# Kernel optimization log

Hardware: AMD Instinct MI355X
Metric: run time of the kernel (lower is better)

Reference implementation:

```python
import jax, jax.numpy as jnp
import numpy as np

B, D, NH, HD = 32, 384, 8, 48
HP = WP = 14
N = HP * WP
L = 24
EPS_LN = 1e-5


def _ln(x, w, b):
    m = jnp.mean(x, -1, keepdims=True)
    v = jnp.mean((x - m) ** 2, -1, keepdims=True)
    return (x - m) * jax.lax.rsqrt(v + EPS_LN) * w + b


def _gelu(x):
    return jax.nn.gelu(x, approximate=False)


def _conv(x, w, s, p, groups=1):
    return jax.lax.conv_general_dilated(x, w, (s, s), [(p, p), (p, p)],
        dimension_numbers=('NCHW', 'OIHW', 'NCHW'), feature_group_count=groups)


def _bn(x, g, b):
    # eval-mode BatchNorm2d with running_mean=0, running_var=1
    scale = g * jax.lax.rsqrt(jnp.asarray(1.0 + 1e-5, x.dtype))
    return x * scale[None, :, None, None] + b[None, :, None, None]


def _pos_embed(pos_w, pos_b):
    two_pi = 2.0 * np.pi
    y = (jnp.arange(HP, dtype=jnp.float32) + 1.0) / ((HP + 1e-6) * two_pi)
    xg = (jnp.arange(WP, dtype=jnp.float32) + 1.0) / ((WP + 1e-6) * two_pi)
    y_embed = jnp.broadcast_to(y[:, None], (HP, WP))
    x_embed = jnp.broadcast_to(xg[None, :], (HP, WP))
    dim_t = 10000.0 ** (2.0 * (jnp.arange(32) // 2).astype(jnp.float32) / 32.0)
    px = x_embed[..., None] / dim_t  # [H,W,32]
    py = y_embed[..., None] / dim_t
    px = jnp.stack([jnp.sin(px[..., 0::2]), jnp.cos(px[..., 1::2])], -1).reshape(HP, WP, 32)
    py = jnp.stack([jnp.sin(py[..., 0::2]), jnp.cos(py[..., 1::2])], -1).reshape(HP, WP, 32)
    pos = jnp.concatenate([py, px], -1)  # [H,W,64]
    pos = jnp.einsum('hwc,dc->hwd', pos, pos_w[:, :, 0, 0]) + pos_b
    return pos.reshape(1, N, D)


def _xca_block(t, p):
    Bc = t.shape[0]
    h = _ln(t, p['n1_w'], p['n1_b'])
    qkv = (h @ p['qkv_w'].T + p['qkv_b']).reshape(Bc, N, 3, NH, HD)
    q = qkv[:, :, 0].transpose(0, 2, 3, 1)  # [B,H,d,N]
    k = qkv[:, :, 1].transpose(0, 2, 3, 1)
    v = qkv[:, :, 2].transpose(0, 2, 3, 1)
    q = q / jnp.maximum(jnp.linalg.norm(q, axis=-1, keepdims=True), 1e-12)
    k = k / jnp.maximum(jnp.linalg.norm(k, axis=-1, keepdims=True), 1e-12)
    attn = jnp.einsum('bhdn,bhen->bhde', q, k) * p['temp'][None, :, None, None]
    a = jax.nn.softmax(attn, -1)  # channel-wise softmax over d_h
    o = jnp.einsum('bhde,bhen->bnhd', a, v).reshape(Bc, N, D)
    o = o @ p['proj_w'].T + p['proj_b']
    t = t + p['g1'] * o
    h = _ln(t, p['n3_w'], p['n3_b']).transpose(0, 2, 1).reshape(Bc, D, HP, WP)
    h = _conv(h, p['lpi1_w'], 1, 1, groups=D) + p['lpi1_b'][None, :, None, None]
    h = _bn(_gelu(h), p['lpi_bn_g'], p['lpi_bn_b'])
    h = _conv(h, p['lpi2_w'], 1, 1, groups=D) + p['lpi2_b'][None, :, None, None]
    t = t + p['g3'] * h.reshape(Bc, D, N).transpose(0, 2, 1)
    h = _ln(t, p['n2_w'], p['n2_b'])
    h = _gelu(h @ p['fc1_w'].T + p['fc1_b']) @ p['fc2_w'].T + p['fc2_b']
    return t + p['g2'] * h


def _ca_block(t, p):
    Bc, Nc, _ = t.shape
    h = _ln(t, p['n1_w'], p['n1_b'])
    qkv = (h @ p['qkv_w'].T + p['qkv_b']).reshape(Bc, Nc, 3, NH, HD)
    q = qkv[:, :, 0].transpose(0, 2, 1, 3)  # [B,H,N,d]
    k = qkv[:, :, 1].transpose(0, 2, 1, 3)
    v = qkv[:, :, 2].transpose(0, 2, 1, 3)
    attn = jnp.sum(q[:, :, :1] * k, -1) * (HD ** -0.5)  # [B,H,N]
    a = jax.nn.softmax(attn, -1)
    cls = jnp.einsum('bhn,bhnd->bhd', a, v).reshape(Bc, 1, D)
    cls = cls @ p['proj_w'].T + p['proj_b']
    attn_out = jnp.concatenate([cls, h[:, 1:]], 1)
    t = t + p['g1'] * attn_out
    t = _ln(t, p['n2_w'], p['n2_b'])
    res = t
    cls2 = _gelu(t[:, :1] @ p['fc1_w'].T + p['fc1_b']) @ p['fc2_w'].T + p['fc2_b']
    return jnp.concatenate([p['g2'] * cls2, t[:, 1:]], 1) + res


def setup_inputs() -> dict:
    key = jax.random.key(0)
    k = iter(jax.random.split(key, 64))
    def rn(shape, std=0.02):
        return jax.random.normal(next(k), shape, jnp.float32) * std
    inp = {}
    inp['x'] = jax.random.normal(next(k), (B, 3, 224, 224), jnp.float32)
    inp['cls_token'] = rn((1, 1, D))
    inp['pos_w'] = rn((D, 64, 1, 1))
    inp['pos_b'] = jnp.zeros((D,))
    for i, (co, ci) in enumerate([(48, 3), (96, 48), (192, 96), (384, 192)], 1):
        inp['pe_w%d' % i] = rn((co, ci, 3, 3))
        inp['pe_g%d' % i] = jnp.ones((co,))
        inp['pe_b%d' % i] = jnp.zeros((co,))
    inp['xqkv_w'] = rn((L, 3 * D, D)); inp['xqkv_b'] = jnp.zeros((L, 3 * D))
    inp['xproj_w'] = rn((L, D, D)); inp['xproj_b'] = jnp.zeros((L, D))
    inp['xtemp'] = jnp.ones((L, NH))
    for n in ('n1', 'n2', 'n3'):
        inp['x%s_w' % n] = jnp.ones((L, D)); inp['x%s_b' % n] = jnp.zeros((L, D))
    inp['xfc1_w'] = rn((L, 4 * D, D)); inp['xfc1_b'] = jnp.zeros((L, 4 * D))
    inp['xfc2_w'] = rn((L, D, 4 * D)); inp['xfc2_b'] = jnp.zeros((L, D))
    inp['xlpi1_w'] = rn((L, D, 1, 3, 3), 0.1); inp['xlpi1_b'] = jnp.zeros((L, D))
    inp['xlpi2_w'] = rn((L, D, 1, 3, 3), 0.1); inp['xlpi2_b'] = jnp.zeros((L, D))
    inp['xbn_g'] = jnp.ones((L, D)); inp['xbn_b'] = jnp.zeros((L, D))
    for g in ('g1', 'g2', 'g3'):
        inp['x%s' % g] = jnp.full((L, D), 1e-5)
    L2 = 2
    inp['cqkv_w'] = rn((L2, 3 * D, D)); inp['cqkv_b'] = jnp.zeros((L2, 3 * D))
    inp['cproj_w'] = rn((L2, D, D)); inp['cproj_b'] = jnp.zeros((L2, D))
    for n in ('n1', 'n2'):
        inp['c%s_w' % n] = jnp.ones((L2, D)); inp['c%s_b' % n] = jnp.zeros((L2, D))
    inp['cfc1_w'] = rn((L2, 4 * D, D)); inp['cfc1_b'] = jnp.zeros((L2, 4 * D))
    inp['cfc2_w'] = rn((L2, D, 4 * D)); inp['cfc2_b'] = jnp.zeros((L2, D))
    inp['cg1'] = jnp.full((L2, D), 1e-5); inp['cg2'] = jnp.full((L2, D), 1e-5)
    inp['norm_w'] = jnp.ones((D,)); inp['norm_b'] = jnp.zeros((D,))
    inp['head_w'] = rn((1000, D)); inp['head_b'] = jnp.zeros((1000,))
    return inp


def reference(x, cls_token, pos_w, pos_b, pe_w1, pe_g1, pe_b1, pe_w2, pe_g2, pe_b2, pe_w3, pe_g3, pe_b3, pe_w4, pe_g4, pe_b4, xqkv_w, xqkv_b, xproj_w, xproj_b, xtemp, xn1_w, xn1_b, xn2_w, xn2_b, xn3_w, xn3_b, xfc1_w, xfc1_b, xfc2_w, xfc2_b, xlpi1_w, xlpi1_b, xlpi2_w, xlpi2_b, xbn_g, xbn_b, xg1, xg2, xg3, cqkv_w, cqkv_b, cproj_w, cproj_b, cn1_w, cn1_b, cn2_w, cn2_b, cfc1_w, cfc1_b, cfc2_w, cfc2_b, cg1, cg2, norm_w, norm_b, head_w, head_b):
    h = _gelu(_bn(_conv(x, pe_w1, 2, 1), pe_g1, pe_b1))
    h = _gelu(_bn(_conv(h, pe_w2, 2, 1), pe_g2, pe_b2))
    h = _gelu(_bn(_conv(h, pe_w3, 2, 1), pe_g3, pe_b3))
    h = _bn(_conv(h, pe_w4, 2, 1), pe_g4, pe_b4)  # [B,D,14,14]
    t = h.reshape(h.shape[0], D, N).transpose(0, 2, 1)  # [B,N,D]
    t = t + _pos_embed(pos_w, pos_b)
    xca = {'qkv_w': xqkv_w, 'qkv_b': xqkv_b, 'proj_w': xproj_w, 'proj_b': xproj_b,
           'temp': xtemp, 'n1_w': xn1_w, 'n1_b': xn1_b, 'n2_w': xn2_w, 'n2_b': xn2_b,
           'n3_w': xn3_w, 'n3_b': xn3_b, 'fc1_w': xfc1_w, 'fc1_b': xfc1_b,
           'fc2_w': xfc2_w, 'fc2_b': xfc2_b, 'lpi1_w': xlpi1_w, 'lpi1_b': xlpi1_b,
           'lpi2_w': xlpi2_w, 'lpi2_b': xlpi2_b, 'lpi_bn_g': xbn_g, 'lpi_bn_b': xbn_b,
           'g1': xg1, 'g2': xg2, 'g3': xg3}
    t, _ = jax.lax.scan(lambda c, p: (_xca_block(c, p), None), t, xca)
    t = jnp.concatenate([jnp.broadcast_to(cls_token, (t.shape[0], 1, D)), t], 1)
    for i in range(2):
        p = {'qkv_w': cqkv_w[i], 'qkv_b': cqkv_b[i], 'proj_w': cproj_w[i],
             'proj_b': cproj_b[i], 'n1_w': cn1_w[i], 'n1_b': cn1_b[i],
             'n2_w': cn2_w[i], 'n2_b': cn2_b[i], 'fc1_w': cfc1_w[i],
             'fc1_b': cfc1_b[i], 'fc2_w': cfc2_w[i], 'fc2_b': cfc2_b[i],
             'g1': cg1[i], 'g2': cg2[i]}
        t = _ca_block(t, p)
    t = _ln(t, norm_w, norm_b)[:, 0]
    return t @ head_w.T + head_b
```

## Files before the change

kernel.cpp:

```cpp
#include <hip/hip_runtime.h>
#include <hip/hip_bf16.h>

#define B_ 32
#define D_ 384
#define N_ 196
#define NH_ 8
#define HD_ 48
#define L_ 24

typedef __bf16 bf16x8 __attribute__((ext_vector_type(8)));
typedef float f32x4 __attribute__((ext_vector_type(4)));

__device__ __forceinline__ float gelu_f(float v){
    return 0.5f * v * (1.0f + erff(v * 0.70710678118654752f));
}

__global__ __launch_bounds__(256) void cvt_bf(const float* __restrict__ s, __bf16* __restrict__ d, long n){
    long i = ((long)blockIdx.x * 256 + threadIdx.x) * 8;
    if (i >= n) return;
    float4 a = *reinterpret_cast<const float4*>(s + i);
    float4 b = *reinterpret_cast<const float4*>(s + i + 4);
    bf16x8 r;
    r[0] = (__bf16)a.x; r[1] = (__bf16)a.y; r[2] = (__bf16)a.z; r[3] = (__bf16)a.w;
    r[4] = (__bf16)b.x; r[5] = (__bf16)b.y; r[6] = (__bf16)b.z; r[7] = (__bf16)b.w;
    *reinterpret_cast<bf16x8*>(d + i) = r;
}

__global__ __launch_bounds__(256) void cvt_pad(const float* __restrict__ s, __bf16* __restrict__ d,
                                               int rows, int K, int rows_pad){
    int id = blockIdx.x * 256 + threadIdx.x;
    if (id >= rows_pad * K) return;
    int r = id / K;
    d[id] = (r < rows) ? (__bf16)s[id] : (__bf16)0.f;
}

__global__ __launch_bounds__(256) void wprep(const float* __restrict__ w, __bf16* __restrict__ W2,
                                             int Co, int Ci, int Kpad){
    int id = blockIdx.x * 256 + threadIdx.x;
    if (id >= Co * Kpad) return;
    int co = id / Kpad, k = id - co * Kpad;
    float v = 0.f;
    if (k < 9 * Ci){
        int tap = k / Ci, ci = k - tap * Ci;
// ... 153 lines not shown
    float* yr = y + row * ystride;
    yr[tid]       = (v0 - m) * r * w[tid]       + b[tid];
    yr[tid + 128] = (v1 - m) * r * w[tid + 128] + b[tid + 128];
    yr[tid + 256] = (v2 - m) * r * w[tid + 256] + b[tid + 256];
}

__global__ __launch_bounds__(128) void ln384_bf(const float* __restrict__ x,
                                                const float* __restrict__ w, const float* __restrict__ b,
                                                __bf16* __restrict__ y){
    long row = blockIdx.x;
    int tid = threadIdx.x;
    const float* xr = x + row * 384;
    float v0 = xr[tid], v1 = xr[tid + 128], v2 = xr[tid + 256];
    float s = v0 + v1 + v2;
    float ss = v0 * v0 + v1 * v1 + v2 * v2;
    for (int off = 32; off; off >>= 1){ s += __shfl_down(s, off); ss += __shfl_down(ss, off); }
    __shared__ float rs[2], rss[2];
    if ((tid & 63) == 0){ rs[tid >> 6] = s; rss[tid >> 6] = ss; }
    __syncthreads();
    float S = rs[0] + rs[1], SS = rss[0] + rss[1];
    float m = S * (1.0f / 384.0f);
    float var = SS * (1.0f / 384.0f) - m * m;
    float r = rsqrtf(var + 1e-5f);
    __bf16* yr = y + row * 384;
    yr[tid]       = (__bf16)((v0 - m) * r * w[tid]       + b[tid]);
    yr[tid + 128] = (__bf16)((v1 - m) * r * w[tid + 128] + b[tid + 128]);
    yr[tid + 256] = (__bf16)((v2 - m) * r * w[tid + 256] + b[tid + 256]);
}

__global__ __launch_bounds__(128) void proj_res_lnt(const __bf16* __restrict__ o2,
                                                    const float* __restrict__ g1,
                                                    float* __restrict__ t,
                                                    const float* __restrict__ n3w, const float* __restrict__ n3b,
                                                    float* __restrict__ ht){
    long row = blockIdx.x;
    int tid = threadIdx.x;
    float v[3];
    #pragma unroll
    for (int i = 0; i < 3; i++){
        int c = tid + i * 128;
        long idx = row * 384 + c;
        v[i] = t[idx] + g1[c] * (float)o2[idx];
        t[idx] = v[i];
    }
    float s = v[0] + v[1] + v[2];
    float ss = v[0] * v[0] + v[1] * v[1] + v[2] * v[2];
    for (int off = 32; off; off >>= 1){ s += __shfl_down(s, off); ss += __shfl_down(ss, off); }
    __shared__ float rs[2], rss[2];
    if ((tid & 63) == 0){ rs[tid >> 6] = s; rss[tid >> 6] = ss; }
    __syncthreads();
    float S = rs[0] + rs[1], SS = rss[0] + rss[1];
    float m = S * (1.0f / 384.0f);
    float var = SS * (1.0f / 384.0f) - m * m;
    float r = rsqrtf(var + 1e-5f);
    int b = (int)(row / 196), n = (int)(row % 196);
    float* yb = ht + ((long)b * 384) * 196 + n;
    #pragma unroll
    for (int i = 0; i < 3; i++){
        int c = tid + i * 128;
        yb[(long)c * 196] = (v[i] - m) * r * n3w[c] + n3b[c];
    }
}

__global__ __launch_bounds__(128) void ln2res(float* __restrict__ t,
                                              const __bf16* __restrict__ hadd,
                                              const float* __restrict__ n2w, const float* __restrict__ n2b,
                                              __bf16* __restrict__ h){
    long row = blockIdx.x;
    int tid = threadIdx.x;
    float v[3];
    #pragma unroll
    for (int i = 0; i < 3; i++){
        int c = tid + i * 128;
        long idx = row * 384 + c;
        v[i] = t[idx] + (float)hadd[idx];
        t[idx] = v[i];
    }
    float s = v[0] + v[1] + v[2];
    float ss = v[0] * v[0] + v[1] * v[1] + v[2] * v[2];
    for (int off = 32; off; off >>= 1){ s += __shfl_down(s, off); ss += __shfl_down(ss, off); }
    __shared__ float rs[2], rss[2];
    if ((tid & 63) == 0){ rs[tid >> 6] = s; rss[tid >> 6] = ss; }
    __syncthreads();
    float S = rs[0] + rs[1], SS = rss[0] + rss[1];
    float m = S * (1.0f / 384.0f);
    float var = SS * (1.0f / 384.0f) - m * m;
    float r = rsqrtf(var + 1e-5f);
    __bf16* yr = h + row * 384;
    #pragma unroll
    for (int i = 0; i < 3; i++){
        int c = tid + i * 128;
        yr[c] = (__bf16)((v[i] - m) * r * n2w[c] + n2b[c]);
    }
}

__global__ __launch_bounds__(128) void fc2_res_ln(const __bf16* __restrict__ f2,
                                                  const float* __restrict__ g2,
                                                  float* __restrict__ t,
                                                  const float* __restrict__ n1w, const float* __restrict__ n1b,
                                                  __bf16* __restrict__ h){
    long row = blockIdx.x;
    int tid = threadIdx.x;
    float v[3];
    #pragma unroll
    for (int i = 0; i < 3; i++){
        int c = tid + i * 128;
        long idx = row * 384 + c;
        v[i] = t[idx] + g2[c] * (float)f2[idx];
        t[idx] = v[i];
    }
    float s = v[0] + v[1] + v[2];
    float ss = v[0] * v[0] + v[1] * v[1] + v[2] * v[2];
    for (int off = 32; off; off >>= 1){ s += __shfl_down(s, off); ss += __shfl_down(ss, off); }
    __shared__ float rs[2], rss[2];
    if ((tid & 63) == 0){ rs[tid >> 6] = s; rss[tid >> 6] = ss; }
    __syncthreads();
    float S = rs[0] + rs[1], SS = rss[0] + rss[1];
    float m = S * (1.0f / 384.0f);
    float var = SS * (1.0f / 384.0f) - m * m;
    float r = rsqrtf(var + 1e-5f);
    __bf16* yr = h + row * 384;
    #pragma unroll
    for (int i = 0; i < 3; i++){
        int c = tid + i * 128;
        yr[c] = (__bf16)((v[i] - m) * r * n1w[c] + n1b[c]);
    }
}

template<int MODE, int OUTBF, int ACVT, int GUARD, int SPLITK, int NGUARD>
__global__ __launch_bounds__(256) void gemm_bb2(const void* __restrict__ Av, long lda,
                                                const __bf16* __restrict__ W, int Kw,
                                                const float* __restrict__ bias,
                                                void* __restrict__ Cv, long ldc,
                                                int K, int M, int Ncols){
    __shared__ __align__(16) char smem[15360];
    char* Ab = smem;
    char* Bb = smem + 5120;
    const int tid = threadIdx.x;
    const int lane = tid & 63;
    const int wn = tid >> 6;
    const int row0 = blockIdx.x * 64;
    const int col0 = blockIdx.y * 128;
    const int hi = lane >> 4, lo = lane & 15;
    const int kbase = SPLITK ? blockIdx.z * K : 0;
    const __bf16* Abf = (const __bf16*)Av;
    const float* Af = (const float*)Av;
    const int r_a = tid >> 2, cq_a = tid & 3;
    f32x4 acc[4][2] = {};
    auto loadA = [&](int kk)->bf16x8 {
        bf16x8 va{};
        int grow = row0 + r_a;
        if (!GUARD || grow < M){
            long ai = (long)grow * lda + kk + cq_a * 8;
            if (ACVT){
                float4 a0 = *reinterpret_cast<const float4*>(Af + ai);
                float4 a1 = *reinterpret_cast<const float4*>(Af + ai + 4);
                va[0] = (__bf16)a0.x; va[1] = (__bf16)a0.y; va[2] = (__bf16)a0.z; va[3] = (__bf16)a0.w;
                va[4] = (__bf16)a1.x; va[5] = (__bf16)a1.y; va[6] = (__bf16)a1.z; va[7] = (__bf16)a1.w;
            } else {
                va = *reinterpret_cast<const bf16x8*>(Abf + ai);
            }
        }
        return va;
    };
    auto loadB = [&](int kk, int i)->bf16x8 {
        int p = i * 256 + tid;
        int r = p >> 2, cq = p & 3;
        return *reinterpret_cast<const bf16x8*>(W + (long)(col0 + r) * Kw + kk + cq * 8);
    };
    bf16x8 vaC = loadA(kbase);
    bf16x8 vwC0 = loadB(kbase, 0), vwC1 = loadB(kbase, 1);
    for (int k0 = 0; k0 < K; k0 += 32){
        *reinterpret_cast<bf16x8*>(Ab + r_a * 80 + cq_a * 16) = vaC;
        #pragma unroll
        for (int i = 0; i < 2; i++){
            int p = i * 256 + tid;
            int r = p >> 2, cq = p & 3;
            *reinterpret_cast<bf16x8*>(Bb + r * 80 + cq * 16) = i ? vwC1 : vwC0;
        }
        __syncthreads();
        int kn = kbase + ((k0 + 32 < K) ? k0 + 32 : k0);
        bf16x8 vaN = loadA(kn);
        bf16x8 vwN0 = loadB(kn, 0), vwN1 = loadB(kn, 1);
        bf16x8 af[4], bfr[2];
        #pragma unroll
        for (int m = 0; m < 4; m++)
            af[m] = *reinterpret_cast<const bf16x8*>(Ab + (m * 16 + lo) * 80 + hi * 16);
        #pragma unroll
        for (int n = 0; n < 2; n++)
            bfr[n] = *reinterpret_cast<const bf16x8*>(Bb + (wn * 32 + n * 16 + lo) * 80 + hi * 16);
        #pragma unroll
        for (int m = 0; m < 4; m++)
            #pragma unroll
            for (int n = 0; n < 2; n++)
                acc[m][n] = __builtin_amdgcn_mfma_f32_16x16x32_bf16(af[m], bfr[n], acc[m][n], 0, 0, 0);
        __syncthreads();
        vaC = vaN; vwC0 = vwN0; vwC1 = vwN1;
    }
    float* Cf = (float*)Cv;
    __bf16* Cb = (__bf16*)Cv;
    if (SPLITK) Cf += (long)blockIdx.z * M * ldc;
    #pragma unroll
    for (int m = 0; m < 4; m++){
        #pragma unroll
        for (int n = 0; n < 2; n++){
            int row = row0 + m * 16 + hi * 4;
            int col = col0 + wn * 32 + n * 16 + lo;
            if (NGUARD && col >= Ncols) continue;
            float bv = (MODE == 3) ? 0.f : bias[col];
            #pragma unroll
            for (int j = 0; j < 4; j++){
                if (GUARD && (row + j) >= M) continue;
                float v = acc[m][n][j] + bv;
                if (MODE == 1) v = gelu_f(v);
                long ci = (long)(row + j) * ldc + col;
                if (OUTBF) Cb[ci] = (__bf16)v;
                else Cf[ci] = v;
            }
        }
    }
}

__global__ __launch_bounds__(256) void gemm_bb3(const __bf16* __restrict__ A, long lda,
                                                const __bf16* __restrict__ W, int Kw,
                                                const float* __restrict__ bias,
                                                __bf16* __restrict__ C, long ldc,
                                                int K){
    __shared__ __align__(16) char smem[10240];
    char* Ab = smem;
    char* Bb = smem + 5120;
    const int tid = threadIdx.x;
    const int lane = tid & 63;
    const int wn = tid >> 6;
    const int row0 = blockIdx.x * 64;
    const int col0 = blockIdx.y * 64;
    const int hi = lane >> 4, lo = lane & 15;
    const int r_s = tid >> 2, cq_s = tid & 3;
    f32x4 acc[4] = {};
    auto loadA = [&](int kk)->bf16x8 {
        return *reinterpret_cast<const bf16x8*>(A + (long)(row0 + r_s) * lda + kk + cq_s * 8);
    };
    auto loadB = [&](int kk)->bf16x8 {
        return *reinterpret_cast<const bf16x8*>(W + (long)(col0 + r_s) * Kw + kk + cq_s * 8);
    };
    bf16x8 vaC = loadA(0);
    bf16x8 vwC = loadB(0);
    for (int k0 = 0; k0 < K; k0 += 32){
        *reinterpret_cast<bf16x8*>(Ab + r_s * 80 + cq_s * 16) = vaC;
        *reinterpret_cast<bf16x8*>(Bb + r_s * 80 + cq_s * 16) = vwC;
        __syncthreads();
        int kn = (k0 + 32 < K) ? k0 + 32 : k0;
        bf16x8 vaN = loadA(kn);
        bf16x8 vwN = loadB(kn);
        bf16x8 af[4], bfr;
        #pragma unroll
        for (int m = 0; m < 4; m++)
            af[m] = *reinterpret_cast<const bf16x8*>(Ab + (m * 16 + lo) * 80 + hi * 16);
        bfr = *reinterpret_cast<const bf16x8*>(Bb + (wn * 16 + lo) * 80 + hi * 16);
        #pragma unroll
        for (int m = 0; m < 4; m++)
            acc[m] = __builtin_amdgcn_mfma_f32_16x16x32_bf16(af[m], bfr, acc[m], 0, 0, 0);
        __syncthreads();
        vaC = vaN; vwC = vwN;
    }
    #pragma unroll
    for (int m = 0; m < 4; m++){
        int row = row0 + m * 16 + hi * 4;
        int col = col0 + wn * 16 + lo;
        float bv = bias[col];
        #pragma unroll
        for (int j = 0; j < 4; j++)
            C[(long)(row + j) * ldc + col] = (__bf16)(acc[m][j] + bv);
    }
}

__global__ __launch_bounds__(384) void pos_embed(const float* __restrict__ pw, const float* __restrict__ pb,
                                                 float* __restrict__ pos){
    __shared__ float p64[64];
    int n = blockIdx.x;
    int iy = n / 14, ix = n % 14;
    int t = threadIdx.x;
    if (t < 64){
        int axis = t >> 5;
        int c = t & 31;
        int u = c >> 1;
        float coord = (axis == 0) ? (float)(iy + 1) : (float)(ix + 1);
        float val = coord / ((14.0f + 1e-6f) * 6.283185307179586f);
        float T = powf(10000.0f, (float)u / 16.0f);
        float a = val / T;
        p64[t] = (c & 1) ? cosf(a) : sinf(a);
    }
    __syncthreads();
    float acc = 0.f;
    const float* wr = pw + (long)t * 64;
    #pragma unroll 8
    for (int c = 0; c < 64; c++) acc += p64[c] * wr[c];
// ... 131 lines not shown
        sm += __shfl_xor(sm, 2);
        float inv = 1.0f / sm;
        #pragma unroll
        for (int i = 0; i < 12; i++) abf[r * 72 + q4 * 12 + i] = (__bf16)(pv[i] * inv);
    }
    for (int idx = tid; idx < 48 * 3; idx += 256){
        int r = idx / 3, c = 48 + (idx % 3) * 8;
        *reinterpret_cast<bf16x8*>(abf + r * 72 + c) = z8;
    }
    __syncthreads();
    __bf16* ob = o + ((long)b * 196) * 384 + h * 48;
    __builtin_amdgcn_s_setprio(1);
    for (int tt = wid; tt < 39; tt += 4){
        int mi = tt / 13, ni = tt % 13;
        f32x4 acc = {};
        #pragma unroll
        for (int e0 = 0; e0 < 64; e0 += 32){
            bf16x8 af = *reinterpret_cast<const bf16x8*>(abf + (mi * 16 + lo) * 72 + e0 + hi * 8);
            bf16x8 bf = *reinterpret_cast<const bf16x8*>(vt + (ni * 16 + lo) * 72 + e0 + hi * 8);
            acc = __builtin_amdgcn_mfma_f32_16x16x32_bf16(af, bf, acc, 0, 0, 0);
        }
        int n = ni * 16 + lo;
        if (n < 196){
            #pragma unroll
            for (int j = 0; j < 4; j++){
                int d = mi * 16 + hi * 4 + j;
                ob[(long)n * 384 + d] = (__bf16)acc[j];
            }
        }
    }
    __builtin_amdgcn_s_setprio(0);
}

__global__ __launch_bounds__(256) void lpi_g(const float* __restrict__ ht,
                                             const float* __restrict__ w1, const float* __restrict__ b1,
                                             const float* __restrict__ bng, const float* __restrict__ bnb,
                                             const float* __restrict__ w2, const float* __restrict__ b2,
                                             const float* __restrict__ g3, __bf16* __restrict__ hadd){
    int bd = blockIdx.x;
    int d = bd % 384, b = bd / 384;
    __shared__ float p[16][16];
    __shared__ float p2[16][16];
    __shared__ float wA[9], wB[9];
    int tt = threadIdx.x;
    int yy = tt / 16, xx = tt % 16;
    p[yy][xx] = 0.f; p2[yy][xx] = 0.f;
    if (tt < 9){ wA[tt] = w1[d * 9 + tt]; wB[tt] = w2[d * 9 + tt]; }
    __syncthreads();
    if (tt < 196){
        int y = tt / 14, x = tt % 14;
        p[y + 1][x + 1] = ht[((long)b * 384 + d) * 196 + tt];
    }
    __syncthreads();
    if (tt < 196){
        int y = tt / 14, x = tt % 14;
        float a = 0.f;
        #pragma unroll
        for (int ky = 0; ky < 3; ky++)
            #pragma unroll
            for (int kx = 0; kx < 3; kx++)
                a += wA[ky * 3 + kx] * p[y + ky][x + kx];
        a += b1[d];
        a = gelu_f(a);
        a = a * (bng[d] * rsqrtf(1.0f + 1e-5f)) + bnb[d];
        p2[y + 1][x + 1] = a;
    }
    __syncthreads();
    if (tt < 196){
        int y = tt / 14, x = tt % 14;
        float a = 0.f;
        #pragma unroll
        for (int ky = 0; ky < 3; ky++)
            #pragma unroll
            for (int kx = 0; kx < 3; kx++)
                a += wB[ky * 3 + kx] * p2[y + ky][x + kx];
        a += b2[d];
        hadd[((long)b * 196 + tt) * 384 + d] = (__bf16)(g3[d] * a);
    }
}

__global__ __launch_bounds__(256) void concat_cls(const float* __restrict__ t, const float* __restrict__ clstok,
                                                  float* __restrict__ tc){
    long i = (long)blockIdx.x * 256 + threadIdx.x;
    if (i >= (long)B_ * 197 * 384) return;
// ... 114 lines not shown
    const float* cfc1_b = (const float*)d_in[49];
    const float* cfc2_w = (const float*)d_in[50];
    const float* cfc2_b = (const float*)d_in[51];
    const float* cg1 = (const float*)d_in[52];
    const float* cg2 = (const float*)d_in[53];
    const float* norm_w = (const float*)d_in[54];
    const float* norm_b = (const float*)d_in[55];
    const float* head_w = (const float*)d_in[56];
    const float* head_b = (const float*)d_in[57];
    float* outp = (float*)d_out;

    float* ws = (float*)d_ws;
    __bf16* A1   = (__bf16*)(ws);
    __bf16* A2   = (__bf16*)(ws);
    __bf16* A3   = (__bf16*)(ws);
    __bf16* A4   = (__bf16*)(ws);
    __bf16* out1 = (__bf16*)(ws + 22500000L);
    __bf16* out2 = (__bf16*)(ws + 22500000L);
    __bf16* out3 = (__bf16*)(ws + 27400000L);
    __bf16* wcv  = (__bf16*)(ws + 36000000L);
    __bf16* W1c = wcv;
    __bf16* W2c = wcv + 1536;
    __bf16* W3c = wcv + 44544;
    __bf16* W4c = wcv + 216576;
    __bf16* wqkv_bf = (__bf16*)(ws);
    __bf16* wproj_bf = (__bf16*)(ws + 5308416L);
    __bf16* wfc1_bf = (__bf16*)(ws + 7077888L);
    __bf16* wfc2_bf = (__bf16*)(ws + 14155776L);
    float*  t       = ws + 21233664L;
    float*  pos     = ws + 23642112L;
    __bf16* h_bf    = (__bf16*)(ws + 23717376L);
    __bf16* qkv_bf  = (__bf16*)(ws + 24921600L);
    __bf16* o_bf    = (__bf16*)(ws + 28534272L);
    float*  ht      = ws + 29738496L;
    __bf16* f1_bf   = (__bf16*)(ws + 32146944L);
    __bf16* o2_bf   = (__bf16*)(ws + 34555392L);
    __bf16* f2_bf   = (__bf16*)(ws + 24921600L);
    __bf16* hadd_bf = (__bf16*)(ws + 28534272L);
    float* tc   = ws;
    float* hc   = ws + 2420736L;
    __bf16* qkvc_bf = (__bf16*)(ws + 4841472L);
    float* clsp = ws + 8472576L;
    float* clso = clsp + 12288;
    float* f1c  = clso + 12288;
    float* cls2 = f1c + 49152;
    float* clsf = cls2 + 12288;
    __bf16* cqkv_bf  = (__bf16*)(ws + 9000000L);
    __bf16* cproj_bf = (__bf16*)(ws + 9500000L);
    __bf16* cfc1_bf  = (__bf16*)(ws + 9800000L);
    __bf16* cfc2_bf  = (__bf16*)(ws + 10400000L);
    __bf16* headw_bf = (__bf16*)(ws + 11000000L);

    wprep<<<(48 * 32 + 255) / 256, 256, 0, stream>>>(pe_w[0], W1c, 48, 3, 32);
    wprep<<<(96 * 448 + 255) / 256, 256, 0, stream>>>(pe_w[1], W2c, 96, 48, 448);
    wprep<<<(192 * 896 + 255) / 256, 256, 0, stream>>>(pe_w[2], W3c, 192, 96, 896);
    wprep<<<(384 * 1728 + 255) / 256, 256, 0, stream>>>(pe_w[3], W4c, 384, 192, 1728);

    im2col_x<<<1568, 256, 0, stream>>>(x, A1);
    { dim3 g(3136, 1); gemm_conv<1, 0><<<g, 256, 0, stream>>>(A1, 32, W1c, pe_g[0], pe_b[0], out1, 48, nullptr); }
    im2col_bf<<<(100352 * 9 + 255) / 256, 256, 0, stream>>>(out1, A2, 48, 112, 112, 56, 56, 448, 100352 * 9);
    { dim3 g(784, 1); gemm_conv<1, 0><<<g, 256, 0, stream>>>(A2, 448, W2c, pe_g[1], pe_b[1], out2, 96, nullptr); }
    im2col_bf<<<(25088 * 9 + 255) / 256, 256, 0, stream>>>(out2, A3, 96, 56, 56, 28, 28, 896, 25088 * 9);
    pos_embed<<<196, 384, 0, stream>>>(pos_w, pos_b, pos);
    { dim3 g(196, 2); gemm_conv<1, 0><<<g, 256, 0, stream>>>(A3, 896, W3c, pe_g[2], pe_b[2], out3, 192, nullptr); }
    im2col_bf<<<(6272 * 9 + 255) / 256, 256, 0, stream>>>(out3, A4, 192, 28, 28, 14, 14, 1728, 6272 * 9);
    { dim3 g(49, 3); gemm_conv<0, 1><<<g, 256, 0, stream>>>(A4, 1728, W4c, pe_g[3], pe_b[3], t, 384, pos); }

    {
        long n1 = (long)L_ * 1152 * 384;
        long n2 = (long)L_ * 384 * 384;
        long n3 = (long)L_ * 1536 * 384;
        cvt_bf<<<(int)((n1 + 2047) / 2048), 256, 0, stream>>>(xqkv_w, wqkv_bf, n1);
        cvt_bf<<<(int)((n2 + 2047) / 2048), 256, 0, stream>>>(xproj_w, wproj_bf, n2);
        cvt_bf<<<(int)((n3 + 2047) / 2048), 256, 0, stream>>>(xfc1_w, wfc1_bf, n3);
        cvt_bf<<<(int)((n3 + 2047) / 2048), 256, 0, stream>>>(xfc2_w, wfc2_bf, n3);
    }

    const int M = B_ * N_;
    ln384_bf<<<M, 128, 0, stream>>>(t, xn1_w, xn1_b, h_bf);
    for (int l = 0; l < L_; l++){
        {
            dim3 g(98, 9);
            gemm_bb2<0, 1, 0, 0, 0, 0><<<g, 256, 0, stream>>>(h_bf, 384, wqkv_bf + (long)l * 1152 * 384, 384,
                                                              xqkv_b + l * 1152, qkv_bf, 1152, 384, M, 0);
        }
        xca2<<<B_ * NH_, 256, 0, stream>>>(qkv_bf, xtemp + l * 8, o_bf);
        {
            dim3 g(98, 6);
            gemm_bb3<<<g, 256, 0, stream>>>(o_bf, 384, wproj_bf + (long)l * 384 * 384, 384,
                                            xproj_b + l * 384, o2_bf, 384, 384);
        }
        proj_res_lnt<<<M, 128, 0, stream>>>(o2_bf, xg1 + l * 384, t,
                                            xn3_w + l * 384, xn3_b + l * 384, ht);
        lpi_g<<<B_ * D_, 256, 0, stream>>>(ht, xlpi1_w + (long)l * 384 * 9, xlpi1_b + l * 384,
                                           xbn_g + l * 384, xbn_b + l * 384,
                                           xlpi2_w + (long)l * 384 * 9, xlpi2_b + l * 384,
                                           xg3 + l * 384, hadd_bf);
        ln2res<<<M, 128, 0, stream>>>(t, hadd_bf, xn2_w + l * 384, xn2_b + l * 384, h_bf);
        {
            dim3 g(98, 12);
            gemm_bb2<1, 1, 0, 0, 0, 0><<<g, 256, 0, stream>>>(h_bf, 384, wfc1_bf + (long)l * 1536 * 384, 384,
                                                              xfc1_b + l * 1536, f1_bf, 1536, 384, M, 0);
        }
        {
            dim3 g(98, 6);
            gemm_bb3<<<g, 256, 0, stream>>>(f1_bf, 1536, wfc2_bf + (long)l * 1536 * 384, 1536,
                                            xfc2_b + l * 384, f2_bf, 384, 1536);
        }
        int ln = (l + 1) % L_;
        fc2_res_ln<<<M, 128, 0, stream>>>(f2_bf, xg2 + l * 384, t,
                                          xn1_w + ln * 384, xn1_b + ln * 384, h_bf);
    }

    const long NC = (long)B_ * 197 * 384;
    concat_cls<<<(int)(NC / 256), 256, 0, stream>>>(t, clstok, tc);
    {
        long nc = (long)2 * 1152 * 384;
        cvt_bf<<<(int)((nc + 2047) / 2048), 256, 0, stream>>>(cqkv_w, cqkv_bf, nc);
        long np = (long)2 * 384 * 384;
        cvt_bf<<<(int)((np + 2047) / 2048), 256, 0, stream>>>(cproj_w, cproj_bf, np);
        long nf = (long)2 * 1536 * 384;
        cvt_bf<<<(int)((nf + 2047) / 2048), 256, 0, stream>>>(cfc1_w, cfc1_bf, nf);
        cvt_bf<<<(int)((nf + 2047) / 2048), 256, 0, stream>>>(cfc2_w, cfc2_bf, nf);
        cvt_pad<<<(1024 * 384 + 255) / 256, 256, 0, stream>>>(head_w, headw_bf, 1000, 384, 1024);
    }
    const int MC = B_ * 197;
    for (int i = 0; i < 2; i++){
        ln384<<<MC, 128, 0, stream>>>(tc, 384, cn1_w + i * 384, cn1_b + i * 384, hc, 384);
        {
            dim3 g(99, 9);
            gemm_bb2<0, 1, 1, 1, 0, 0><<<g, 256, 0, stream>>>(hc, 384, cqkv_bf + (long)i * 1152 * 384, 384,
                                                              cqkv_b + i * 1152, qkvc_bf, 1152, 384, MC, 0);
        }
        ca_attn<<<B_ * NH_, 256, 0, stream>>>(qkvc_bf, clsp);
        {
            dim3 g(1, 3);
            gemm_bb2<0, 0, 1, 1, 0, 0><<<g, 256, 0, stream>>>(clsp, 384, cproj_bf + (long)i * 384 * 384, 384,
                                                              cproj_b + i * 384, clso, 384, 384, 32, 0);
        }
        ca_update1<<<(int)(NC / 256), 256, 0, stream>>>(clso, hc, cg1 + i * 384, tc);
        ln384<<<MC, 128, 0, stream>>>(tc, 384, cn2_w + i * 384, cn2_b + i * 384, hc, 384);
        {
            dim3 g(1, 12);
            gemm_bb2<1, 0, 1, 1, 0, 0><<<g, 256, 0, stream>>>(hc, (long)197 * 384, cfc1_bf + (long)i * 1536 * 384, 384,
                                                              cfc1_b + i * 1536, f1c, 1536, 384, 32, 0);
        }
        {
            dim3 g(1, 3);
            gemm_bb2<0, 0, 1, 1, 0, 0><<<g, 256, 0, stream>>>(f1c, 1536, cfc2_bf + (long)i * 1536 * 384, 1536,
                                                              cfc2_b + i * 384, cls2, 384, 1536, 32, 0);
        }
        ca_update2<<<(int)(NC / 256), 256, 0, stream>>>(cls2, hc, cg2 + i * 384, tc);
    }

    ln384<<<32, 128, 0, stream>>>(tc, (long)197 * 384, norm_w, norm_b, clsf, 384);
    {
        dim3 g(1, 8);
        gemm_bb2<0, 0, 1, 1, 0, 1><<<g, 256, 0, stream>>>(clsf, 384, headw_bf, 384,
                                                          head_b, outp, 1000, 384, 32, 1000);
    }
}
```

Measured before the change: 4.188 ms.

## Double GEMM K-tile to 64, vectorize LN kernels, store LPI input as bf16

```diff
diff --git a/kernel.cpp b/kernel.cpp
--- a/kernel.cpp
+++ b/kernel.cpp
@@ -9,6 +9,7 @@
 #define L_ 24
 
 typedef __bf16 bf16x8 __attribute__((ext_vector_type(8)));
+typedef __bf16 bf16x4 __attribute__((ext_vector_type(4)));
 typedef float f32x4 __attribute__((ext_vector_type(4)));
 
 __device__ __forceinline__ float gelu_f(float v){
@@ -228,19 +229,22 @@
                                                     const float* __restrict__ g1,
                                                     float* __restrict__ t,
                                                     const float* __restrict__ n3w, const float* __restrict__ n3b,
-                                                    float* __restrict__ ht){
+                                                    __bf16* __restrict__ ht){
     long row = blockIdx.x;
     int tid = threadIdx.x;
-    float v[3];
-    #pragma unroll
-    for (int i = 0; i < 3; i++){
-        int c = tid + i * 128;
-        long idx = row * 384 + c;
-        v[i] = t[idx] + g1[c] * (float)o2[idx];
-        t[idx] = v[i];
-    }
-    float s = v[0] + v[1] + v[2];
-    float ss = v[0] * v[0] + v[1] * v[1] + v[2] * v[2];
+    int c0 = tid * 4;
+    float v[4] = {0.f, 0.f, 0.f, 0.f};
+    if (tid < 96){
+        float4 tv = *reinterpret_cast<const float4*>(t + row * 384 + c0);
+        bf16x4 ov = *reinterpret_cast<const bf16x4*>(o2 + row * 384 + c0);
+        v[0] = tv.x + g1[c0 + 0] * (float)ov[0];
+        v[1] = tv.y + g1[c0 + 1] * (float)ov[1];
+        v[2] = tv.z + g1[c0 + 2] * (float)ov[2];
+        v[3] = tv.w + g1[c0 + 3] * (float)ov[3];
+        *reinterpret_cast<float4*>(t + row * 384 + c0) = make_float4(v[0], v[1], v[2], v[3]);
+    }
+    float s = v[0] + v[1] + v[2] + v[3];
+    float ss = v[0] * v[0] + v[1] * v[1] + v[2] * v[2] + v[3] * v[3];
     for (int off = 32; off; off >>= 1){ s += __shfl_down(s, off); ss += __shfl_down(ss, off); }
     __shared__ float rs[2], rss[2];
     if ((tid & 63) == 0){ rs[tid >> 6] = s; rss[tid >> 6] = ss; }
@@ -249,12 +253,14 @@
     float m = S * (1.0f / 384.0f);
     float var = SS * (1.0f / 384.0f) - m * m;
     float r = rsqrtf(var + 1e-5f);
-    int b = (int)(row / 196), n = (int)(row % 196);
-    float* yb = ht + ((long)b * 384) * 196 + n;
-    #pragma unroll
-    for (int i = 0; i < 3; i++){
-        int c = tid + i * 128;
-        yb[(long)c * 196] = (v[i] - m) * r * n3w[c] + n3b[c];
+    if (tid < 96){
+        int b = (int)(row / 196), n = (int)(row % 196);
+        __bf16* yb = ht + ((long)b * 384) * 196 + n;
+        #pragma unroll
+        for (int j = 0; j < 4; j++){
+            int c = c0 + j;
+            yb[(long)c * 196] = (__bf16)((v[j] - m) * r * n3w[c] + n3b[c]);
+        }
     }
 }
 
@@ -264,16 +270,19 @@
                                               __bf16* __restrict__ h){
     long row = blockIdx.x;
     int tid = threadIdx.x;
-    float v[3];
-    #pragma unroll
-    for (int i = 0; i < 3; i++){
-        int c = tid + i * 128;
-        long idx = row * 384 + c;
-        v[i] = t[idx] + (float)hadd[idx];
-        t[idx] = v[i];
-    }
-    float s = v[0] + v[1] + v[2];
-    float ss = v[0] * v[0] + v[1] * v[1] + v[2] * v[2];
+    int c0 = tid * 4;
+    float v[4] = {0.f, 0.f, 0.f, 0.f};
+    if (tid < 96){
+        float4 tv = *reinterpret_cast<const float4*>(t + row * 384 + c0);
+        bf16x4 hv = *reinterpret_cast<const bf16x4*>(hadd + row * 384 + c0);
+        v[0] = tv.x + (float)hv[0];
+        v[1] = tv.y + (float)hv[1];
+        v[2] = tv.z + (float)hv[2];
+        v[3] = tv.w + (float)hv[3];
+        *reinterpret_cast<float4*>(t + row * 384 + c0) = make_float4(v[0], v[1], v[2], v[3]);
+    }
+    float s = v[0] + v[1] + v[2] + v[3];
+    float ss = v[0] * v[0] + v[1] * v[1] + v[2] * v[2] + v[3] * v[3];
     for (int off = 32; off; off >>= 1){ s += __shfl_down(s, off); ss += __shfl_down(ss, off); }
     __shared__ float rs[2], rss[2];
     if ((tid & 63) == 0){ rs[tid >> 6] = s; rss[tid >> 6] = ss; }
@@ -282,11 +291,14 @@
     float m = S * (1.0f / 384.0f);
     float var = SS * (1.0f / 384.0f) - m * m;
     float r = rsqrtf(var + 1e-5f);
-    __bf16* yr = h + row * 384;
-    #pragma unroll
-    for (int i = 0; i < 3; i++){
-        int c = tid + i * 128;
-        yr[c] = (__bf16)((v[i] - m) * r * n2w[c] + n2b[c]);
+    if (tid < 96){
+        bf16x4 o;
+        #pragma unroll
+        for (int j = 0; j < 4; j++){
+            int c = c0 + j;
+            o[j] = (__bf16)((v[j] - m) * r * n2w[c] + n2b[c]);
+        }
+        *reinterpret_cast<bf16x4*>(h + row * 384 + c0) = o;
     }
 }
 
@@ -297,16 +309,19 @@
                                                   __bf16* __restrict__ h){
     long row = blockIdx.x;
     int tid = threadIdx.x;
-    float v[3];
-    #pragma unroll
-    for (int i = 0; i < 3; i++){
-        int c = tid + i * 128;
-        long idx = row * 384 + c;
-        v[i] = t[idx] + g2[c] * (float)f2[idx];
-        t[idx] = v[i];
-    }
-    float s = v[0] + v[1] + v[2];
-    float ss = v[0] * v[0] + v[1] * v[1] + v[2] * v[2];
+    int c0 = tid * 4;
+    float v[4] = {0.f, 0.f, 0.f, 0.f};
+    if (tid < 96){
+        float4 tv = *reinterpret_cast<const float4*>(t + row * 384 + c0);
+        bf16x4 fv = *reinterpret_cast<const bf16x4*>(f2 + row * 384 + c0);
+        v[0] = tv.x + g2[c0 + 0] * (float)fv[0];
+        v[1] = tv.y + g2[c0 + 1] * (float)fv[1];
+        v[2] = tv.z + g2[c0 + 2] * (float)fv[2];
+        v[3] = tv.w + g2[c0 + 3] * (float)fv[3];
+        *reinterpret_cast<float4*>(t + row * 384 + c0) = make_float4(v[0], v[1], v[2], v[3]);
+    }
+    float s = v[0] + v[1] + v[2] + v[3];
+    float ss = v[0] * v[0] + v[1] * v[1] + v[2] * v[2] + v[3] * v[3];
     for (int off = 32; off; off >>= 1){ s += __shfl_down(s, off); ss += __shfl_down(ss, off); }
     __shared__ float rs[2], rss[2];
     if ((tid & 63) == 0){ rs[tid >> 6] = s; rss[tid >> 6] = ss; }
@@ -315,39 +330,42 @@
     float m = S * (1.0f / 384.0f);
     float var = SS * (1.0f / 384.0f) - m * m;
     float r = rsqrtf(var + 1e-5f);
-    __bf16* yr = h + row * 384;
-    #pragma unroll
-    for (int i = 0; i < 3; i++){
-        int c = tid + i * 128;
-        yr[c] = (__bf16)((v[i] - m) * r * n1w[c] + n1b[c]);
-    }
-}
-
-template<int MODE, int OUTBF, int ACVT, int GUARD, int SPLITK, int NGUARD>
+    if (tid < 96){
+        bf16x4 o;
+        #pragma unroll
+        for (int j = 0; j < 4; j++){
+            int c = c0 + j;
+            o[j] = (__bf16)((v[j] - m) * r * n1w[c] + n1b[c]);
+        }
+        *reinterpret_cast<bf16x4*>(h + row * 384 + c0) = o;
+    }
+}
+
+template<int MODE, int OUTBF, int ACVT, int GUARD, int NGUARD>
 __global__ __launch_bounds__(256) void gemm_bb2(const void* __restrict__ Av, long lda,
                                                 const __bf16* __restrict__ W, int Kw,
                                                 const float* __restrict__ bias,
                                                 void* __restrict__ Cv, long ldc,
                                                 int K, int M, int Ncols){
-    __shared__ __align__(16) char smem[15360];
+    __shared__ __align__(16) char smem[27648];
     char* Ab = smem;
-    char* Bb = smem + 5120;
+    char* Bb = smem + 9216;
     const int tid = threadIdx.x;
     const int lane = tid & 63;
     const int wn = tid >> 6;
     const int row0 = blockIdx.x * 64;
     const int col0 = blockIdx.y * 128;
     const int hi = lane >> 4, lo = lane & 15;
-    const int kbase = SPLITK ? blockIdx.z * K : 0;
     const __bf16* Abf = (const __bf16*)Av;
     const float* Af = (const float*)Av;
-    const int r_a = tid >> 2, cq_a = tid & 3;
     f32x4 acc[4][2] = {};
-    auto loadA = [&](int kk)->bf16x8 {
+    auto loadA = [&](int kk, int i)->bf16x8 {
+        int p = i * 256 + tid;
+        int r = p >> 3, cq = p & 7;
         bf16x8 va{};
-        int grow = row0 + r_a;
+        int grow = row0 + r;
         if (!GUARD || grow < M){
-            long ai = (long)grow * lda + kk + cq_a * 8;
+            long ai = (long)grow * lda + kk + cq * 8;
             if (ACVT){
                 float4 a0 = *reinterpret_cast<const float4*>(Af + ai);
                 float4 a1 = *reinterpret_cast<const float4*>(Af + ai + 4);
@@ -361,41 +379,57 @@
     };
     auto loadB = [&](int kk, int i)->bf16x8 {
         int p = i * 256 + tid;
-        int r = p >> 2, cq = p & 3;
+        int r = p >> 3, cq = p & 7;
         return *reinterpret_cast<const bf16x8*>(W + (long)(col0 + r) * Kw + kk + cq * 8);
     };
-    bf16x8 vaC = loadA(kbase);
-    bf16x8 vwC0 = loadB(kbase, 0), vwC1 = loadB(kbase, 1);
-    for (int k0 = 0; k0 < K; k0 += 32){
-        *reinterpret_cast<bf16x8*>(Ab + r_a * 80 + cq_a * 16) = vaC;
+    bf16x8 vaC[2], vwC[4];
+    vaC[0] = loadA(0, 0); vaC[1] = loadA(0, 1);
+    #pragma unroll
+    for (int i = 0; i < 4; i++) vwC[i] = loadB(0, i);
+    for (int k0 = 0; k0 < K; k0 += 64){
         #pragma unroll
         for (int i = 0; i < 2; i++){
             int p = i * 256 + tid;
-            int r = p >> 2, cq = p & 3;
-            *reinterpret_cast<bf16x8*>(Bb + r * 80 + cq * 16) = i ? vwC1 : vwC0;
+            int r = p >> 3, cq = p & 7;
+            *reinterpret_cast<bf16x8*>(Ab + r * 144 + cq * 16) = vaC[i];
+        }
+        #pragma unroll
+        for (int i = 0; i < 4; i++){
+            int p = i * 256 + tid;
+            int r = p >> 3, cq = p & 7;
+            *reinterpret_cast<bf16x8*>(Bb + r * 144 + cq * 16) = vwC[i];
         }
         __syncthreads();
-        int kn = kbase + ((k0 + 32 < K) ? k0 + 32 : k0);
-        bf16x8 vaN = loadA(kn);
-        bf16x8 vwN0 = loadB(kn, 0), vwN1 = loadB(kn, 1);
-        bf16x8 af[4], bfr[2];
-        #pragma unroll
-        for (int m = 0; m < 4; m++)
-            af[m] = *reinterpret_cast<const bf16x8*>(Ab + (m * 16 + lo) * 80 + hi * 16);
-        #pragma unroll
-        for (int n = 0; n < 2; n++)
-            bfr[n] = *reinterpret_cast<const bf16x8*>(Bb + (wn * 32 + n * 16 + lo) * 80 + hi * 16);
-        #pragma unroll
-        for (int m = 0; m < 4; m++)
+        int kn = (k0 + 64 < K) ? k0 + 64 : k0;
+        bf16x8 vaN[2], vwN[4];
+        vaN[0] = loadA(kn, 0); vaN[1] = loadA(kn, 1);
+        #pragma unroll
+        for (int i = 0; i < 4; i++) vwN[i] = loadB(kn, i);
+        bf16x8 af[2][4], bfr[2][2];
+        #pragma unroll
+        for (int m = 0; m < 4; m++){
+            af[0][m] = *reinterpret_cast<const bf16x8*>(Ab + (m * 16 + lo) * 144 + hi * 16);
+            af[1][m] = *reinterpret_cast<const bf16x8*>(Ab + (m * 16 + lo) * 144 + 64 + hi * 16);
+        }
+        #pragma unroll
+        for (int n = 0; n < 2; n++){
+            bfr[0][n] = *reinterpret_cast<const bf16x8*>(Bb + (wn * 32 + n * 16 + lo) * 144 + hi * 16);
+            bfr[1][n] = *reinterpret_cast<const bf16x8*>(Bb + (wn * 32 + n * 16 + lo) * 144 + 64 + hi * 16);
+        }
+        #pragma unroll
+        for (int kc = 0; kc < 2; kc++)
             #pragma unroll
-            for (int n = 0; n < 2; n++)
-                acc[m][n] = __builtin_amdgcn_mfma_f32_16x16x32_bf16(af[m], bfr[n], acc[m][n], 0, 0, 0);
+            for (int m = 0; m < 4; m++)
+                #pragma unroll
+                for (int n = 0; n < 2; n++)
+                    acc[m][n] = __builtin_amdgcn_mfma_f32_16x16x32_bf16(af[kc][m], bfr[kc][n], acc[m][n], 0, 0, 0);
         __syncthreads();
-        vaC = vaN; vwC0 = vwN0; vwC1 = vwN1;
+        vaC[0] = vaN[0]; vaC[1] = vaN[1];
+        #pragma unroll
+        for (int i = 0; i < 4; i++) vwC[i] = vwN[i];
     }
     float* Cf = (float*)Cv;
     __bf16* Cb = (__bf16*)Cv;
-    if (SPLITK) Cf += (long)blockIdx.z * M * ldc;
     #pragma unroll
     for (int m = 0; m < 4; m++){
         #pragma unroll
@@ -403,7 +437,7 @@
             int row = row0 + m * 16 + hi * 4;
             int col = col0 + wn * 32 + n * 16 + lo;
             if (NGUARD && col >= Ncols) continue;
-            float bv = (MODE == 3) ? 0.f : bias[col];
+            float bv = bias[col];
             #pragma unroll
             for (int j = 0; j < 4; j++){
                 if (GUARD && (row + j) >= M) continue;
@@ -422,42 +456,57 @@
                                                 const float* __restrict__ bias,
                                                 __bf16* __restrict__ C, long ldc,
                                                 int K){
-    __shared__ __align__(16) char smem[10240];
+    __shared__ __align__(16) char smem[18432];
     char* Ab = smem;
-    char* Bb = smem + 5120;
+    char* Bb = smem + 9216;
     const int tid = threadIdx.x;
     const int lane = tid & 63;
     const int wn = tid >> 6;
     const int row0 = blockIdx.x * 64;
     const int col0 = blockIdx.y * 64;
     const int hi = lane >> 4, lo = lane & 15;
-    const int r_s = tid >> 2, cq_s = tid & 3;
     f32x4 acc[4] = {};
-    auto loadA = [&](int kk)->bf16x8 {
-        return *reinterpret_cast<const bf16x8*>(A + (long)(row0 + r_s) * lda + kk + cq_s * 8);
+    auto loadA = [&](int kk, int i)->bf16x8 {
+        int p = i * 256 + tid;
+        int r = p >> 3, cq = p & 7;
+        return *reinterpret_cast<const bf16x8*>(A + (long)(row0 + r) * lda + kk + cq * 8);
     };
-    auto loadB = [&](int kk)->bf16x8 {
-        return *reinterpret_cast<const bf16x8*>(W + (long)(col0 + r_s) * Kw + kk + cq_s * 8);
+    auto loadB = [&](int kk, int i)->bf16x8 {
+        int p = i * 256 + tid;
+        int r = p >> 3, cq = p & 7;
+        return *reinterpret_cast<const bf16x8*>(W + (long)(col0 + r) * Kw + kk + cq * 8);
     };
-    bf16x8 vaC = loadA(0);
-    bf16x8 vwC = loadB(0);
-    for (int k0 = 0; k0 < K; k0 += 32){
-        *reinterpret_cast<bf16x8*>(Ab + r_s * 80 + cq_s * 16) = vaC;
-        *reinterpret_cast<bf16x8*>(Bb + r_s * 80 + cq_s * 16) = vwC;
+    bf16x8 vaC[2], vwC[2];
+    vaC[0] = loadA(0, 0); vaC[1] = loadA(0, 1);
+    vwC[0] = loadB(0, 0); vwC[1] = loadB(0, 1);
+    for (int k0 = 0; k0 < K; k0 += 64){
+        #pragma unroll
+        for (int i = 0; i < 2; i++){
+            int p = i * 256 + tid;
+            int r = p >> 3, cq = p & 7;
+            *reinterpret_cast<bf16x8*>(Ab + r * 144 + cq * 16) = vaC[i];
+            *reinterpret_cast<bf16x8*>(Bb + r * 144 + cq * 16) = vwC[i];
+        }
         __syncthreads();
-        int kn = (k0 + 32 < K) ? k0 + 32 : k0;
-        bf16x8 vaN = loadA(kn);
-        bf16x8 vwN = loadB(kn);
-        bf16x8 af[4], bfr;
-        #pragma unroll
-        for (int m = 0; m < 4; m++)
-            af[m] = *reinterpret_cast<const bf16x8*>(Ab + (m * 16 + lo) * 80 + hi * 16);
-        bfr = *reinterpret_cast<const bf16x8*>(Bb + (wn * 16 + lo) * 80 + hi * 16);
-        #pragma unroll
-        for (int m = 0; m < 4; m++)
-            acc[m] = __builtin_amdgcn_mfma_f32_16x16x32_bf16(af[m], bfr, acc[m], 0, 0, 0);
+        int kn = (k0 + 64 < K) ? k0 + 64 : k0;
+        bf16x8 vaN[2], vwN[2];
+        vaN[0] = loadA(kn, 0); vaN[1] = loadA(kn, 1);
+        vwN[0] = loadB(kn, 0); vwN[1] = loadB(kn, 1);
+        bf16x8 af[2][4], bfr[2];
+        #pragma unroll
+        for (int m = 0; m < 4; m++){
+            af[0][m] = *reinterpret_cast<const bf16x8*>(Ab + (m * 16 + lo) * 144 + hi * 16);
+            af[1][m] = *reinterpret_cast<const bf16x8*>(Ab + (m * 16 + lo) * 144 + 64 + hi * 16);
+        }
+        bfr[0] = *reinterpret_cast<const bf16x8*>(Bb + (wn * 16 + lo) * 144 + hi * 16);
+        bfr[1] = *reinterpret_cast<const bf16x8*>(Bb + (wn * 16 + lo) * 144 + 64 + hi * 16);
+        #pragma unroll
+        for (int kc = 0; kc < 2; kc++)
+            #pragma unroll
+            for (int m = 0; m < 4; m++)
+                acc[m] = __builtin_amdgcn_mfma_f32_16x16x32_bf16(af[kc][m], bfr[kc], acc[m], 0, 0, 0);
         __syncthreads();
-        vaC = vaN; vwC = vwN;
+        vaC[0] = vaN[0]; vaC[1] = vaN[1]; vwC[0] = vwN[0]; vwC[1] = vwN[1];
     }
     #pragma unroll
     for (int m = 0; m < 4; m++){
@@ -655,7 +704,7 @@
     __builtin_amdgcn_s_setprio(0);
 }
 
-__global__ __launch_bounds__(256) void lpi_g(const float* __restrict__ ht,
+__global__ __launch_bounds__(256) void lpi_g(const __bf16* __restrict__ ht,
                                              const float* __restrict__ w1, const float* __restrict__ b1,
                                              const float* __restrict__ bng, const float* __restrict__ bnb,
                                              const float* __restrict__ w2, const float* __restrict__ b2,
@@ -672,7 +721,7 @@
     __syncthreads();
     if (tt < 196){
         int y = tt / 14, x = tt % 14;
-        p[y + 1][x + 1] = ht[((long)b * 384 + d) * 196 + tt];
+        p[y + 1][x + 1] = (float)ht[((long)b * 384 + d) * 196 + tt];
     }
     __syncthreads();
     if (tt < 196){
@@ -853,7 +902,7 @@
     __bf16* h_bf    = (__bf16*)(ws + 23717376L);
     __bf16* qkv_bf  = (__bf16*)(ws + 24921600L);
     __bf16* o_bf    = (__bf16*)(ws + 28534272L);
-    float*  ht      = ws + 29738496L;
+    __bf16* ht_bf   = (__bf16*)(ws + 29738496L);
     __bf16* f1_bf   = (__bf16*)(ws + 32146944L);
     __bf16* o2_bf   = (__bf16*)(ws + 34555392L);
     __bf16* f2_bf   = (__bf16*)(ws + 24921600L);
@@ -902,8 +951,8 @@
     for (int l = 0; l < L_; l++){
         {
             dim3 g(98, 9);
-            gemm_bb2<0, 1, 0, 0, 0, 0><<<g, 256, 0, stream>>>(h_bf, 384, wqkv_bf + (long)l * 1152 * 384, 384,
-                                                              xqkv_b + l * 1152, qkv_bf, 1152, 384, M, 0);
+            gemm_bb2<0, 1, 0, 0, 0><<<g, 256, 0, stream>>>(h_bf, 384, wqkv_bf + (long)l * 1152 * 384, 384,
+                                                           xqkv_b + l * 1152, qkv_bf, 1152, 384, M, 0);
         }
         xca2<<<B_ * NH_, 256, 0, stream>>>(qkv_bf, xtemp + l * 8, o_bf);
         {
@@ -912,16 +961,16 @@
                                             xproj_b + l * 384, o2_bf, 384, 384);
         }
         proj_res_lnt<<<M, 128, 0, stream>>>(o2_bf, xg1 + l * 384, t,
-                                            xn3_w + l * 384, xn3_b + l * 384, ht);
-        lpi_g<<<B_ * D_, 256, 0, stream>>>(ht, xlpi1_w + (long)l * 384 * 9, xlpi1_b + l * 384,
+                                            xn3_w + l * 384, xn3_b + l * 384, ht_bf);
+        lpi_g<<<B_ * D_, 256, 0, stream>>>(ht_bf, xlpi1_w + (long)l * 384 * 9, xlpi1_b + l * 384,
                                            xbn_g + l * 384, xbn_b + l * 384,
                                            xlpi2_w + (long)l * 384 * 9, xlpi2_b + l * 384,
                                            xg3 + l * 384, hadd_bf);
         ln2res<<<M, 128, 0, stream>>>(t, hadd_bf, xn2_w + l * 384, xn2_b + l * 384, h_bf);
         {
             dim3 g(98, 12);
-            gemm_bb2<1, 1, 0, 0, 0, 0><<<g, 256, 0, stream>>>(h_bf, 384, wfc1_bf + (long)l * 1536 * 384, 384,
-                                                              xfc1_b + l * 1536, f1_bf, 1536, 384, M, 0);
+            gemm_bb2<1, 1, 0, 0, 0><<<g, 256, 0, stream>>>(h_bf, 384, wfc1_bf + (long)l * 1536 * 384, 384,
+                                                           xfc1_b + l * 1536, f1_bf, 1536, 384, M, 0);
         }
         {
             dim3 g(98, 6);
@@ -950,26 +999,26 @@
         ln384<<<MC, 128, 0, stream>>>(tc, 384, cn1_w + i * 384, cn1_b + i * 384, hc, 384);
         {
             dim3 g(99, 9);
-            gemm_bb2<0, 1, 1, 1, 0, 0><<<g, 256, 0, stream>>>(hc, 384, cqkv_bf + (long)i * 1152 * 384, 384,
-                                                              cqkv_b + i * 1152, qkvc_bf, 1152, 384, MC, 0);
+            gemm_bb2<0, 1, 1, 1, 0><<<g, 256, 0, stream>>>(hc, 384, cqkv_bf + (long)i * 1152 * 384, 384,
+                                                           cqkv_b + i * 1152, qkvc_bf, 1152, 384, MC, 0);
         }
         ca_attn<<<B_ * NH_, 256, 0, stream>>>(qkvc_bf, clsp);
         {
             dim3 g(1, 3);
-            gemm_bb2<0, 0, 1, 1, 0, 0><<<g, 256, 0, stream>>>(clsp, 384, cproj_bf + (long)i * 384 * 384, 384,
-                                                              cproj_b + i * 384, clso, 384, 384, 32, 0);
+            gemm_bb2<0, 0, 1, 1, 0><<<g, 256, 0, stream>>>(clsp, 384, cproj_bf + (long)i * 384 * 384, 384,
+                                                           cproj_b + i * 384, clso, 384, 384, 32, 0);
         }
         ca_update1<<<(int)(NC / 256), 256, 0, stream>>>(clso, hc, cg1 + i * 384, tc);
         ln384<<<MC, 128, 0, stream>>>(tc, 384, cn2_w + i * 384, cn2_b + i * 384, hc, 384);
         {
             dim3 g(1, 12);
-            gemm_bb2<1, 0, 1, 1, 0, 0><<<g, 256, 0, stream>>>(hc, (long)197 * 384, cfc1_bf + (long)i * 1536 * 384, 384,
-                                                              cfc1_b + i * 1536, f1c, 1536, 384, 32, 0);
+            gemm_bb2<1, 0, 1, 1, 0><<<g, 256, 0, stream>>>(hc, (long)197 * 384, cfc1_bf + (long)i * 1536 * 384, 384,
+                                                           cfc1_b + i * 1536, f1c, 1536, 384, 32, 0);
         }
         {
             dim3 g(1, 3);
-            gemm_bb2<0, 0, 1, 1, 0, 0><<<g, 256, 0, stream>>>(f1c, 1536, cfc2_bf + (long)i * 1536 * 384, 1536,
-                                                              cfc2_b + i * 384, cls2, 384, 1536, 32, 0);
+            gemm_bb2<0, 0, 1, 1, 0><<<g, 256, 0, stream>>>(f1c, 1536, cfc2_bf + (long)i * 1536 * 384, 1536,
+                                                           cfc2_b + i * 384, cls2, 384, 1536, 32, 0);
         }
         ca_update2<<<(int)(NC / 256), 256, 0, stream>>>(cls2, hc, cg2 + i * 384, tc);
     }
@@ -977,7 +1026,7 @@
     ln384<<<32, 128, 0, stream>>>(tc, (long)197 * 384, norm_w, norm_b, clsf, 384);
     {
         dim3 g(1, 8);
-        gemm_bb2<0, 0, 1, 1, 0, 1><<<g, 256, 0, stream>>>(clsf, 384, headw_bf, 384,
-                                                          head_b, outp, 1000, 384, 32, 1000);
-    }
-}
+        gemm_bb2<0, 0, 1, 1, 1><<<g, 256, 0, stream>>>(clsf, 384, headw_bf, 384,
+                                                       head_b, outp, 1000, 384, 32, 1000);
+    }
+}
```

After: 3.966 ms. 1.06x faster.
